# Kernel tuning notes

Measured on AMD Instinct MI355X. Metric: run time of the kernel, lower is better.

## Reference

```python
import jax, jax.numpy as jnp
import numpy as np

# Poincare ball hyperbolic multi-head attention (hypll-style HMultiheadAttention)
C = 1.0          # ball curvature
SQRT_C = 1.0
EPS = 1e-7
B, S, E, H = 4, 1024, 512, 8
HD = E // H      # head_dim = 64


def _project_to_ball(u, scale=0.5):
    n = jnp.linalg.norm(u, axis=-1, keepdims=True)
    return u * (scale / (1.0 + n))  # guarantees ||x|| < scale < 1/sqrt(C)


def h_linear(x, z, r):
    """Poincare fully-connected layer (Shimizu et al. HNN++), as in hypll HLinear.
    x: [..., n] points in the ball, z: [n, m] weight directions, r: [m] bias."""
    x2 = jnp.sum(x * x, -1, keepdims=True)
    lam = 2.0 / jnp.maximum(1.0 - C * x2, EPS)          # conformal factor lambda_x
    zn = jnp.maximum(jnp.linalg.norm(z, axis=0), EPS)    # [m]
    xz = x @ z                                           # [..., m]
    two_cr = 2.0 * SQRT_C * r
    v = (2.0 * zn / SQRT_C) * jnp.arcsinh(
        SQRT_C * lam * xz / zn * jnp.cosh(two_cr) - (lam - 1.0) * jnp.sinh(two_cr)
    )
    v2 = jnp.sum(v * v, -1, keepdims=True)
    return v / (1.0 + jnp.sqrt(1.0 + C * v2))            # map back into the ball


def _split_heads(x):
    b, s, e = x.shape
    return x.reshape(b, s, H, HD).transpose(0, 2, 1, 3)  # [B,H,S,hd]; matches split(dim=-1)


def _h_attention(q, k, v):
    # similarity = -poincare_dist(q, k), pairwise via the arccosh closed form
    # (avoids materializing a [B,H,Sq,Sk,hd] mobius_add tensor)
    q2 = jnp.sum(q * q, -1)[..., :, None]                # [B,H,Sq,1]
    k2 = jnp.sum(k * k, -1)[..., None, :]                # [B,H,1,Sk]
    qk = jnp.einsum('bhqd,bhkd->bhqk', q, k)
    diff2 = jnp.maximum(q2 + k2 - 2.0 * qk, 0.0)
    denom = jnp.maximum((1.0 - C * q2) * (1.0 - C * k2), EPS)
    arg = 1.0 + 2.0 * C * diff2 / denom
    dist = jnp.arccosh(jnp.maximum(arg, 1.0 + EPS)) / SQRT_C
    w = jax.nn.softmax(-dist, axis=-1)                   # attention_activation
    # attention_midpoint: weighted Mobius gyromidpoint then half scalar-mul
    v2 = jnp.sum(v * v, -1)                              # [B,H,Sk]
    lam = 2.0 / jnp.maximum(1.0 - C * v2, EPS)
    num = jnp.einsum('bhqk,bhkd->bhqd', w * lam[..., None, :], v)
    den = jnp.einsum('bhqk,bhk->bhq', w, lam - 1.0)[..., None]
    m_bar = num / jnp.where(jnp.abs(den) < EPS, EPS, den)
    mn = jnp.maximum(jnp.linalg.norm(m_bar, axis=-1, keepdims=True), EPS)
    t = jnp.minimum(SQRT_C * mn, 1.0 - 1e-6)
    return jnp.tanh(0.5 * jnp.arctanh(t)) * m_bar / (SQRT_C * mn)  # (1/2) mobius-scalar-mul


def setup_inputs() -> dict:
    key = jax.random.key(0)
    ks = jax.random.split(key, 9)
    query = _project_to_ball(jax.random.normal(ks[0], (B, S, E), jnp.float32))
    key_t = _project_to_ball(jax.random.normal(ks[1], (B, S, E), jnp.float32))
    value = _project_to_ball(jax.random.normal(ks[2], (B, S, E), jnp.float32))
    scale = E ** -0.5
    zq = jax.random.normal(ks[3], (E, E), jnp.float32) * scale
    zk = jax.random.normal(ks[4], (E, E), jnp.float32) * scale
    zv = jax.random.normal(ks[5], (E, E), jnp.float32) * scale
    rq = jax.random.normal(ks[6], (E,), jnp.float32) * 0.01
    rk = jax.random.normal(ks[7], (E,), jnp.float32) * 0.01
    rv = jax.random.normal(ks[8], (E,), jnp.float32) * 0.01
    return {"query": query, "key": key_t, "value": value,
            "zq": zq, "rq": rq, "zk": zk, "rk": rk, "zv": zv, "rv": rv}


def reference(query, key, value, zq, rq, zk, rk, zv, rv):
    pq = h_linear(query, zq, rq)
    pk = h_linear(key, zk, rk)
    pv = h_linear(value, zv, rv)
    q, k, v = _split_heads(pq), _split_heads(pk), _split_heads(pv)
    out = _h_attention(q, k, v)                          # [B,H,S,hd]
    return out.transpose(0, 2, 1, 3).reshape(B, S, E)    # manifold.cat over heads
```

## Files before the change

### kernel.cpp

```cpp
#include <hip/hip_runtime.h>
#include <math.h>

#define EPSf 1e-7f
typedef unsigned short u16;
typedef __attribute__((ext_vector_type(8))) short bf16x8;
typedef __attribute__((ext_vector_type(4))) float f32x4;

__device__ __forceinline__ float bf2f(u16 u) {
  union { unsigned int i; float f; } x; x.i = ((unsigned int)u) << 16; return x.f;
}
__device__ __forceinline__ u16 f2bf(float f) {
  union { float f; unsigned int i; } x; x.f = f;
  unsigned int r = x.i + 0x7fffu + ((x.i >> 16) & 1u);
  return (u16)(r >> 16);
}
__device__ __forceinline__ void gll16(const void* g, void* l) {
  __builtin_amdgcn_global_load_lds((__attribute__((address_space(1))) void*)(g),
                                   (__attribute__((address_space(3))) void*)(l),
                                   16, 0, 0);
}

__global__ __launch_bounds__(256) void split_z(
    const float* __restrict__ zq, const float* __restrict__ zk, const float* __restrict__ zv,
    const float* __restrict__ rq, const float* __restrict__ rk, const float* __restrict__ rv,
    u16* __restrict__ ZhT, u16* __restrict__ ZlT, float4* __restrict__ WM) {
  const int mat = blockIdx.x >> 3;
  const int c0 = (blockIdx.x & 7) * 64;
  const float* Z = (mat == 0) ? zq : (mat == 1) ? zk : zv;
  const float* R = (mat == 0) ? rq : (mat == 1) ? rk : rv;
  __shared__ float tile[64][68];
  const int t = threadIdx.x;
  const int cl = t >> 2, kg4 = t & 3;
  const size_t zo = (size_t)mat * 512 * 512;
  float csum = 0.f;
  for (int kt = 0; kt < 8; ++kt) {
    __syncthreads();
    {
      int kl = t >> 2;
      const float* src = Z + (size_t)(kt * 64 + kl) * 512 + c0;
      #pragma unroll
      for (int j = 0; j < 4; ++j) {
        float4 v = *(const float4*)(src + (t & 3) * 16 + 4 * j);
        *(float4*)&tile[kl][(t & 3) * 16 + 4 * j] = v;
      }
    }
    __syncthreads();
    #pragma unroll
    for (int jj = 0; jj < 4; ++jj) {
      u16 hb[4], lb[4];
      #pragma unroll
      for (int qq = 0; qq < 4; ++qq) {
        float zval = tile[kg4 * 16 + jj * 4 + qq][cl];
        csum = fmaf(zval, zval, csum);
        u16 hh = f2bf(zval);
        hb[qq] = hh;
        lb[qq] = f2bf(zval - bf2f(hh));
      }
      size_t o = zo + (size_t)(c0 + cl) * 512 + kt * 64 + kg4 * 16 + jj * 4;
      *(ushort4*)(ZhT + o) = make_ushort4(hb[0], hb[1], hb[2], hb[3]);
      *(ushort4*)(ZlT + o) = make_ushort4(lb[0], lb[1], lb[2], lb[3]);
    }
  }
  csum += __shfl_xor(csum, 1);
  csum += __shfl_xor(csum, 2);
  if (kg4 == 0) {
    float zn = fmaxf(sqrtf(csum), EPSf);
    float tr = 2.f * R[c0 + cl];
    float e = expf(tr), ei = 1.f / e;
    WM[mat * 512 + c0 + cl] = make_float4(0.5f * (e + ei) / zn, 0.5f * (e - ei), 2.f * zn, 0.f);
  }
}

__global__ __launch_bounds__(256) void split_x(
    const float* __restrict__ xq, const float* __restrict__ xk, const float* __restrict__ xv,
    u16* __restrict__ Xh, u16* __restrict__ Xl,
    float* __restrict__ Xn, float* __restrict__ Vn) {
  const int gr = blockIdx.x * 2 + (threadIdx.x >> 7);
  const int mat = gr >> 12, row = gr & 4095;
  const float* X = (mat == 0) ? xq : (mat == 1) ? xk : xv;
  const int f4 = threadIdx.x & 127;
  float4 x = ((const float4*)(X + (size_t)row * 512))[f4];
  u16 h0 = f2bf(x.x), h1 = f2bf(x.y), h2 = f2bf(x.z), h3 = f2bf(x.w);
  u16 l0 = f2bf(x.x - bf2f(h0)), l1 = f2bf(x.y - bf2f(h1));
  u16 l2 = f2bf(x.z - bf2f(h2)), l3 = f2bf(x.w - bf2f(h3));
  ((ushort4*)(Xh + (size_t)gr * 512))[f4] = make_ushort4(h0, h1, h2, h3);
  ((ushort4*)(Xl + (size_t)gr * 512))[f4] = make_ushort4(l0, l1, l2, l3);
  float a = fmaf(x.x, x.x, fmaf(x.y, x.y, fmaf(x.z, x.z, x.w * x.w)));
  a += __shfl_xor(a, 1);  a += __shfl_xor(a, 2);  a += __shfl_xor(a, 4);
  a += __shfl_xor(a, 8);  a += __shfl_xor(a, 16); a += __shfl_xor(a, 32);
  __shared__ float red[4];
  if ((threadIdx.x & 63) == 0) red[threadIdx.x >> 6] = a;
  __syncthreads();
  if (threadIdx.x == 0)   { Xn[gr] = red[0] + red[1]; Vn[gr] = 0.f; }
  if (threadIdx.x == 128) { Xn[gr] = red[2] + red[3]; Vn[gr] = 0.f; }
}

__global__ __launch_bounds__(256) void proj_gemm(
    const u16* __restrict__ Xh, const u16* __restrict__ Xl,
    const u16* __restrict__ ZhT, const u16* __restrict__ ZlT,
    const float* __restrict__ Xn, const float4* __restrict__ WM,
    float* __restrict__ Vtmp, float* __restrict__ Vn) {
  const int m0 = blockIdx.x * 128;
  const int n0 = blockIdx.y * 128;
  const int mat = blockIdx.z;
  const size_t xoff = (size_t)mat * 4096 * 512;
  const size_t zoff = (size_t)mat * 512 * 512;
  const int t = threadIdx.x, wv = t >> 6, lane = t & 63;
  const int l15 = lane & 15, quad = lane >> 4;

  __shared__ __align__(16) u16 Ah[128 * 32], Al[128 * 32], Bh[128 * 32], Bl[128 * 32];
  __shared__ float lams[128], lam1s[128], wmxs[128], wmys[128], wmzs[128];

  if (t < 128) {
    float x2 = Xn[mat * 4096 + m0 + t];
    float lam = 2.f / fmaxf(1.f - x2, EPSf);
    lams[t] = lam; lam1s[t] = lam - 1.f;
    float4 wm = WM[mat * 512 + n0 + t];
    wmxs[t] = wm.x; wmys[t] = wm.y; wmzs[t] = wm.z;
  }

  f32x4 acc[4][4];
  #pragma unroll
  for (int i = 0; i < 4; ++i)
    #pragma unroll
    for (int j = 0; j < 4; ++j) acc[i][j] = (f32x4){0.f, 0.f, 0.f, 0.f};

  const int srow = 32 * wv + (lane >> 2);
  const int scol = (lane & 3) * 8;
  const u16* gAh = Xh + xoff + (size_t)(m0 + srow) * 512 + scol;
  const u16* gAl = Xl + xoff + (size_t)(m0 + srow) * 512 + scol;
  const u16* gBh = ZhT + zoff + (size_t)(n0 + srow) * 512 + scol;
  const u16* gBl = ZlT + zoff + (size_t)(n0 + srow) * 512 + scol;

  for (int k0 = 0; k0 < 512; k0 += 32) {
    __syncthreads();
    gll16(gAh + k0,            &Ah[(32 * wv) * 32]);
    gll16(gAh + k0 + 16 * 512, &Ah[(32 * wv + 16) * 32]);
    gll16(gAl + k0,            &Al[(32 * wv) * 32]);
    gll16(gAl + k0 + 16 * 512, &Al[(32 * wv + 16) * 32]);
    gll16(gBh + k0,            &Bh[(32 * wv) * 32]);
    gll16(gBh + k0 + 16 * 512, &Bh[(32 * wv + 16) * 32]);
    gll16(gBl + k0,            &Bl[(32 * wv) * 32]);
    gll16(gBl + k0 + 16 * 512, &Bl[(32 * wv + 16) * 32]);
    __syncthreads();
    const int mh = (wv >> 1) * 64, nh = (wv & 1) * 64;
    bf16x8 ah[4], al[4], bh_[4], bl_[4];
    #pragma unroll
    for (int i = 0; i < 4; ++i) {
      int ra = mh + i * 16 + l15;
      ah[i] = *(const bf16x8*)&Ah[ra * 32 + quad * 8];
      al[i] = *(const bf16x8*)&Al[ra * 32 + quad * 8];
      int rb = nh + i * 16 + l15;
      bh_[i] = *(const bf16x8*)&Bh[rb * 32 + quad * 8];
      bl_[i] = *(const bf16x8*)&Bl[rb * 32 + quad * 8];
    }
    #pragma unroll
    for (int i = 0; i < 4; ++i)
      #pragma unroll
      for (int j = 0; j < 4; ++j) {
        acc[i][j] = __builtin_amdgcn_mfma_f32_16x16x32_bf16(ah[i], bh_[j], acc[i][j], 0, 0, 0);
        acc[i][j] = __builtin_amdgcn_mfma_f32_16x16x32_bf16(ah[i], bl_[j], acc[i][j], 0, 0, 0);
        acc[i][j] = __builtin_amdgcn_mfma_f32_16x16x32_bf16(al[i], bh_[j], acc[i][j], 0, 0, 0);
      }
  }

  const int mh = (wv >> 1) * 64, nh = (wv & 1) * 64;
  #pragma unroll
  for (int i = 0; i < 4; ++i) {
    float rsum[4] = {0.f, 0.f, 0.f, 0.f};
    #pragma unroll
    for (int j = 0; j < 4; ++j) {
      int nl = nh + j * 16 + l15;
      float wx = wmxs[nl], wy = wmys[nl], wz = wmzs[nl];
      #pragma unroll
      for (int r = 0; r < 4; ++r) {
        int ml = mh + i * 16 + quad * 4 + r;
        float tt = lams[ml] * acc[i][j][r] * wx - lam1s[ml] * wy;
        float v = wz * logf(tt + sqrtf(fmaf(tt, tt, 1.f)));
        Vtmp[xoff + (size_t)(m0 + ml) * 512 + (n0 + nl)] = v;
        rsum[r] = fmaf(v, v, rsum[r]);
      }
    }
    #pragma unroll
    for (int r = 0; r < 4; ++r) {
      rsum[r] += __shfl_xor(rsum[r], 1);
      rsum[r] += __shfl_xor(rsum[r], 2);
      rsum[r] += __shfl_xor(rsum[r], 4);
      rsum[r] += __shfl_xor(rsum[r], 8);
    }
    if (l15 == 0) {
      #pragma unroll
      for (int r = 0; r < 4; ++r)
        atomicAdd(&Vn[mat * 4096 + m0 + mh + i * 16 + quad * 4 + r], rsum[r]);
    }
  }
}

__global__ __launch_bounds__(256) void pack_qk(
    const float* __restrict__ Vtmp, const float* __restrict__ Vn,
    u16* __restrict__ Qh, u16* __restrict__ Kh,
    float* __restrict__ q2a, float* __restrict__ aqa,
    float* __restrict__ k2a, float* __restrict__ cka) {
  const int mat = blockIdx.x >> 7;
  const int rb = blockIdx.x & 127;
  const int r = threadIdx.x >> 3;
  const int h = threadIdx.x & 7;
  const int row = rb * 32 + r;
  const size_t gr = (size_t)mat * 4096 + row;
  const float sc = 1.f / (1.f + sqrtf(1.f + Vn[gr]));
  const float* src = Vtmp + gr * 512 + h * 64;
  const int b = row >> 10, s = row & 1023;
  u16* dst = (mat ? Kh : Qh) + ((size_t)(b * 8 + h) * 1024 + s) * 64;
  float nrm = 0.f;
  #pragma unroll
  for (int j = 0; j < 16; ++j) {
    float4 x = *(const float4*)(src + 4 * j);
    u16 u0 = f2bf(x.x * sc), u1 = f2bf(x.y * sc), u2 = f2bf(x.z * sc), u3 = f2bf(x.w * sc);
    *(ushort4*)(dst + 4 * j) = make_ushort4(u0, u1, u2, u3);
    float f0 = bf2f(u0), f1 = bf2f(u1), f2 = bf2f(u2), f3 = bf2f(u3);
    nrm += f0 * f0 + f1 * f1 + f2 * f2 + f3 * f3;
  }
  const size_t so = (size_t)(b * 8 + h) * 1024 + s;
  if (mat == 0) { q2a[so] = nrm; aqa[so] = 1.f / fmaxf(1.f - nrm, EPSf); }
  else          { k2a[so] = nrm; cka[so] = 2.f / fmaxf(1.f - nrm, EPSf); }
}

__global__ __launch_bounds__(256) void pack_v(
    const float* __restrict__ Vtmp, const float* __restrict__ Vn,
    u16* __restrict__ VTb, float* __restrict__ l1a) {
  const int bh = blockIdx.x >> 4;
  const int st = blockIdx.x & 15;
  const int b = bh >> 3, h = bh & 7;
  __shared__ u16 tile[64][72];
  __shared__ float lams[64];
  const int t = threadIdx.x;
  {
    const int s = t >> 2, dg = t & 3;
    const size_t gr = (size_t)2 * 4096 + b * 1024 + st * 64 + s;
    const float sc = 1.f / (1.f + sqrtf(1.f + Vn[gr]));
    const float* src = Vtmp + gr * 512 + h * 64 + dg * 16;
    float nrm = 0.f;
    #pragma unroll
    for (int j = 0; j < 4; ++j) {
      float4 x = *(const float4*)(src + 4 * j);
      u16 u0 = f2bf(x.x * sc), u1 = f2bf(x.y * sc), u2 = f2bf(x.z * sc), u3 = f2bf(x.w * sc);
      *(ushort4*)&tile[s][dg * 16 + 4 * j] = make_ushort4(u0, u1, u2, u3);
      float f0 = bf2f(u0), f1 = bf2f(u1), f2 = bf2f(u2), f3 = bf2f(u3);
      nrm += f0 * f0 + f1 * f1 + f2 * f2 + f3 * f3;
    }
    nrm += __shfl_xor(nrm, 1);
    nrm += __shfl_xor(nrm, 2);
    if (dg == 0) {
      float lam = 2.f / fmaxf(1.f - nrm, EPSf);
      lams[s] = lam;
      l1a[(size_t)bh * 1024 + st * 64 + s] = lam - 1.f;
    }
  }
  __syncthreads();
  const int d = t >> 2, sg = t & 3;
  u16 ob[16];
  #pragma unroll
  for (int j = 0; j < 16; ++j) {
    int ss = sg * 16 + j;
    ob[j] = f2bf(bf2f(tile[ss][d]) * lams[ss]);
  }
  u16* dst = VTb + ((size_t)bh * 64 + d) * 1024 + st * 64 + sg * 16;
  #pragma unroll
  for (int j = 0; j < 4; ++j)
    *(ushort4*)(dst + 4 * j) = make_ushort4(ob[4 * j], ob[4 * j + 1], ob[4 * j + 2], ob[4 * j + 3]);
}

__global__ __launch_bounds__(256) void attn(
    const u16* __restrict__ Qh, const u16* __restrict__ Kh, const u16* __restrict__ VTb,
    const float* __restrict__ q2a, const float* __restrict__ aqa,
    const float* __restrict__ k2a, const float* __restrict__ cka,
    const float* __restrict__ l1a, float* __restrict__ out) {
  const int bh = blockIdx.y;
  const int b = bh >> 3, h = bh & 7;
  const int q0 = blockIdx.x * 64;
  const int t = threadIdx.x, wv = t >> 6, lane = t & 63;
  const int l15 = lane & 15, quad = lane >> 4;

  __shared__ __align__(16) u16 Qs[64 * 72], Ks[64 * 72], VsT[64 * 72], Ws[64 * 72];
  __shared__ float k2s[64], cks[64], l1s[64], dens[64];

  #pragma unroll
  for (int i = 0; i < 2; ++i) {
    int f = t + 256 * i;
    int row = f >> 3, g = f & 7;
    float4 v = *(const float4*)(Qh + ((size_t)bh * 1024 + q0 + row) * 64 + g * 8);
    *(float4*)&Qs[row * 72 + g * 8] = v;
  }
  float q2r[4], aqr[4];
  #pragma unroll
  for (int r = 0; r < 4; ++r) {
    int qi = bh * 1024 + q0 + 16 * wv + 4 * quad + r;
    q2r[r] = q2a[qi];
    aqr[r] = aqa[qi];
  }
  __syncthreads();
  const bf16x8 qf0 = *(const bf16x8*)&Qs[(16 * wv + l15) * 72 + quad * 8];
  const bf16x8 qf1 = *(const bf16x8*)&Qs[(16 * wv + l15) * 72 + 32 + quad * 8];

  f32x4 num[4];
  #pragma unroll
  for (int i = 0; i < 4; ++i) num[i] = (f32x4){0.f, 0.f, 0.f, 0.f};
  float denp[4] = {0.f, 0.f, 0.f, 0.f};

  for (int kt = 0; kt < 16; ++kt) {
    __syncthreads();
    #pragma unroll
    for (int i = 0; i < 2; ++i) {
      int f = t + 256 * i;
      int row = f >> 3, g = f & 7;
      float4 kv = *(const float4*)(Kh + ((size_t)bh * 1024 + kt * 64 + row) * 64 + g * 8);
      *(float4*)&Ks[row * 72 + g * 8] = kv;
      float4 vv = *(const float4*)(VTb + ((size_t)bh * 64 + row) * 1024 + kt * 64 + g * 8);
      *(float4*)&VsT[row * 72 + g * 8] = vv;
    }
    if (t < 64) {
      int ki = bh * 1024 + kt * 64 + t;
      k2s[t] = k2a[ki]; cks[t] = cka[ki]; l1s[t] = l1a[ki];
    }
    __syncthreads();

    f32x4 sc_[4];
    #pragma unroll
    for (int tn = 0; tn < 4; ++tn) {
      bf16x8 kf0 = *(const bf16x8*)&Ks[(16 * tn + l15) * 72 + quad * 8];
      bf16x8 kf1 = *(const bf16x8*)&Ks[(16 * tn + l15) * 72 + 32 + quad * 8];
      f32x4 s = (f32x4){0.f, 0.f, 0.f, 0.f};
      s = __builtin_amdgcn_mfma_f32_16x16x32_bf16(qf0, kf0, s, 0, 0, 0);
      s = __builtin_amdgcn_mfma_f32_16x16x32_bf16(qf1, kf1, s, 0, 0, 0);
      sc_[tn] = s;
    }
    #pragma unroll
    for (int tn = 0; tn < 4; ++tn) {
      int kidx = 16 * tn + l15;
      float k2 = k2s[kidx], ck = cks[kidx], l1f = l1s[kidx];
      u16 wu[4];
      #pragma unroll
      for (int r = 0; r < 4; ++r) {
        float d2 = fmaxf(fmaf(-2.f, sc_[tn][r], q2r[r] + k2), 0.f);
        float u = fmaxf(d2 * ck * aqr[r], EPSf);
        float s2 = sqrtf(u * (u + 2.f));
        float w = (1.f + u) - s2;
        u16 wb = f2bf(w);
        wu[r] = wb;
        denp[r] = fmaf(bf2f(wb), l1f, denp[r]);
      }
      #pragma unroll
      for (int r = 0; r < 4; ++r)
        Ws[(16 * wv + 4 * quad + r) * 72 + kidx] = wu[r];
    }
    #pragma unroll
    for (int ks = 0; ks < 2; ++ks) {
      bf16x8 wf = *(const bf16x8*)&Ws[(16 * wv + l15) * 72 + ks * 32 + quad * 8];
      #pragma unroll
      for (int tm = 0; tm < 4; ++tm) {
        bf16x8 vf = *(const bf16x8*)&VsT[(16 * tm + l15) * 72 + ks * 32 + quad * 8];
        num[tm] = __builtin_amdgcn_mfma_f32_16x16x32_bf16(vf, wf, num[tm], 0, 0, 0);
      }
    }
  }

  #pragma unroll
  for (int r = 0; r < 4; ++r) {
    denp[r] += __shfl_xor(denp[r], 1);
    denp[r] += __shfl_xor(denp[r], 2);
    denp[r] += __shfl_xor(denp[r], 4);
    denp[r] += __shfl_xor(denp[r], 8);
  }
  if (l15 < 4) {
    float dv = (l15 == 0) ? denp[0] : (l15 == 1) ? denp[1] : (l15 == 2) ? denp[2] : denp[3];
    dens[16 * wv + 4 * quad + l15] = dv;
  }
  float den = dens[16 * wv + l15];
  den = (fabsf(den) < EPSf) ? EPSf : den;
  float inv = 1.f / den;
  float mv[4][4];
  float p = 0.f;
  #pragma unroll
  for (int tm = 0; tm < 4; ++tm)
    #pragma unroll
    for (int r = 0; r < 4; ++r) {
      float m = num[tm][r] * inv;
      mv[tm][r] = m;
      p = fmaf(m, m, p);
    }
  p += __shfl_xor(p, 16);
  p += __shfl_xor(p, 32);
  float mn = sqrtf(p);
  float mnc = fmaxf(mn, EPSf);
  float tt2 = fminf(mnc, 1.f - 1e-6f);
  float scale = tt2 / ((1.f + sqrtf(fmaxf(1.f - tt2 * tt2, 0.f))) * mnc);
  const int qg = b * 1024 + q0 + 16 * wv + l15;
  #pragma unroll
  for (int tm = 0; tm < 4; ++tm) {
    float4 o = make_float4(mv[tm][0] * scale, mv[tm][1] * scale, mv[tm][2] * scale, mv[tm][3] * scale);
    *(float4*)(out + (size_t)qg * 512 + h * 64 + tm * 16 + quad * 4) = o;
  }
}

extern "C" void kernel_launch(void* const* d_in, const int* in_sizes, int n_in,
                              void* d_out, int out_size, void* d_ws, size_t ws_size,
                              hipStream_t stream) {
  (void)in_sizes; (void)n_in; (void)out_size; (void)ws_size;
  const float* q  = (const float*)d_in[0];
  const float* k  = (const float*)d_in[1];
  const float* v  = (const float*)d_in[2];
  const float* zq = (const float*)d_in[3];
  const float* rq = (const float*)d_in[4];
  const float* zk = (const float*)d_in[5];
  const float* rk = (const float*)d_in[6];
  const float* zv = (const float*)d_in[7];
  const float* rv = (const float*)d_in[8];

  unsigned char* ws = (unsigned char*)d_ws;
  u16*   Xh   = (u16*)(ws + 0);
  u16*   Xl   = (u16*)(ws + 12582912);
  u16*   ZhT  = (u16*)(ws + 25165824);
  u16*   ZlT  = (u16*)(ws + 26738688);
  float* Vtmp = (float*)(ws + 28311552);
  float* Xn   = (float*)(ws + 53477376);
  float* Vn   = (float*)(ws + 53526528);
  float4* WM  = (float4*)(ws + 53575680);
  u16*   Qh   = (u16*)(ws + 0);
  u16*   Kh   = (u16*)(ws + 4194304);
  u16*   VTb  = (u16*)(ws + 8388608);
  float* q2a  = (float*)(ws + 12582912);
  float* aqa  = (float*)(ws + 12713984);
  float* k2a  = (float*)(ws + 12845056);
  float* cka  = (float*)(ws + 12976128);
  float* l1a  = (float*)(ws + 13107200);

  split_z<<<24, 256, 0, stream>>>(zq, zk, zv, rq, rk, rv, ZhT, ZlT, WM);
  split_x<<<6144, 256, 0, stream>>>(q, k, v, Xh, Xl, Xn, Vn);
  proj_gemm<<<dim3(32, 4, 3), 256, 0, stream>>>(Xh, Xl, ZhT, ZlT, Xn, WM, Vtmp, Vn);
  pack_qk<<<256, 256, 0, stream>>>(Vtmp, Vn, Qh, Kh, q2a, aqa, k2a, cka);
  pack_v<<<512, 256, 0, stream>>>(Vtmp, Vn, VTb, l1a);
  attn<<<dim3(16, 32), 256, 0, stream>>>(Qh, Kh, VTb, q2a, aqa, k2a, cka, l1a, (float*)d_out);
}
```

Measured before the change: 191.0 us.

## Raise grid parallelism across split_z, projection GEMM and attention; merge pack kernels

split_z now runs 192 blocks, one per k-tile, and accumulates column norms with atomics into a buffer zeroed by split_x. The WM bias terms are computed inside proj_gemm instead. proj_gemm uses 64-row tiles to double its block count, and pack_qk and pack_v merge into a single launch with the per-key scalars interleaved into a float4 array. attn switches to 32-query blocks that split the key range across wave pairs and reduce num and den through shared memory. All of this aims to fill more CUs on small grids and cut launch count, at the cost of atomics, extra shared-memory reductions and more redundant B-tile loads.

```diff
diff --git a/kernel.cpp b/kernel.cpp
--- a/kernel.cpp
+++ b/kernel.cpp
@@ -20,61 +20,14 @@
                                    16, 0, 0);
 }
 
-__global__ __launch_bounds__(256) void split_z(
-    const float* __restrict__ zq, const float* __restrict__ zk, const float* __restrict__ zv,
-    const float* __restrict__ rq, const float* __restrict__ rk, const float* __restrict__ rv,
-    u16* __restrict__ ZhT, u16* __restrict__ ZlT, float4* __restrict__ WM) {
-  const int mat = blockIdx.x >> 3;
-  const int c0 = (blockIdx.x & 7) * 64;
-  const float* Z = (mat == 0) ? zq : (mat == 1) ? zk : zv;
-  const float* R = (mat == 0) ? rq : (mat == 1) ? rk : rv;
-  __shared__ float tile[64][68];
-  const int t = threadIdx.x;
-  const int cl = t >> 2, kg4 = t & 3;
-  const size_t zo = (size_t)mat * 512 * 512;
-  float csum = 0.f;
-  for (int kt = 0; kt < 8; ++kt) {
-    __syncthreads();
-    {
-      int kl = t >> 2;
-      const float* src = Z + (size_t)(kt * 64 + kl) * 512 + c0;
-      #pragma unroll
-      for (int j = 0; j < 4; ++j) {
-        float4 v = *(const float4*)(src + (t & 3) * 16 + 4 * j);
-        *(float4*)&tile[kl][(t & 3) * 16 + 4 * j] = v;
-      }
-    }
-    __syncthreads();
-    #pragma unroll
-    for (int jj = 0; jj < 4; ++jj) {
-      u16 hb[4], lb[4];
-      #pragma unroll
-      for (int qq = 0; qq < 4; ++qq) {
-        float zval = tile[kg4 * 16 + jj * 4 + qq][cl];
-        csum = fmaf(zval, zval, csum);
-        u16 hh = f2bf(zval);
-        hb[qq] = hh;
-        lb[qq] = f2bf(zval - bf2f(hh));
-      }
-      size_t o = zo + (size_t)(c0 + cl) * 512 + kt * 64 + kg4 * 16 + jj * 4;
-      *(ushort4*)(ZhT + o) = make_ushort4(hb[0], hb[1], hb[2], hb[3]);
-      *(ushort4*)(ZlT + o) = make_ushort4(lb[0], lb[1], lb[2], lb[3]);
-    }
-  }
-  csum += __shfl_xor(csum, 1);
-  csum += __shfl_xor(csum, 2);
-  if (kg4 == 0) {
-    float zn = fmaxf(sqrtf(csum), EPSf);
-    float tr = 2.f * R[c0 + cl];
-    float e = expf(tr), ei = 1.f / e;
-    WM[mat * 512 + c0 + cl] = make_float4(0.5f * (e + ei) / zn, 0.5f * (e - ei), 2.f * zn, 0.f);
-  }
-}
-
 __global__ __launch_bounds__(256) void split_x(
     const float* __restrict__ xq, const float* __restrict__ xk, const float* __restrict__ xv,
     u16* __restrict__ Xh, u16* __restrict__ Xl,
-    float* __restrict__ Xn, float* __restrict__ Vn) {
+    float* __restrict__ Xn, float* __restrict__ Vn, float* __restrict__ Zn) {
+  if (blockIdx.x == 0) {
+    #pragma unroll
+    for (int j = 0; j < 6; ++j) Zn[threadIdx.x + 256 * j] = 0.f;
+  }
   const int gr = blockIdx.x * 2 + (threadIdx.x >> 7);
   const int mat = gr >> 12, row = gr & 4095;
   const float* X = (mat == 0) ? xq : (mat == 1) ? xk : xv;
@@ -95,67 +48,122 @@
   if (threadIdx.x == 128) { Xn[gr] = red[2] + red[3]; Vn[gr] = 0.f; }
 }
 
+__global__ __launch_bounds__(256) void split_z(
+    const float* __restrict__ zq, const float* __restrict__ zk, const float* __restrict__ zv,
+    u16* __restrict__ ZhT, u16* __restrict__ ZlT, float* __restrict__ Zn) {
+  const int idx = blockIdx.x;
+  const int mat = idx >> 6;
+  const int cg = (idx >> 3) & 7, kt = idx & 7;
+  const int c0 = cg * 64;
+  const float* Z = (mat == 0) ? zq : (mat == 1) ? zk : zv;
+  __shared__ float tile[64][68];
+  const int t = threadIdx.x;
+  {
+    int kl = t >> 2;
+    const float* src = Z + (size_t)(kt * 64 + kl) * 512 + c0 + (t & 3) * 16;
+    #pragma unroll
+    for (int j = 0; j < 4; ++j) {
+      float4 v = *(const float4*)(src + 4 * j);
+      *(float4*)&tile[kl][(t & 3) * 16 + 4 * j] = v;
+    }
+  }
+  __syncthreads();
+  const int cl = t >> 2, kg4 = t & 3;
+  const size_t zo = (size_t)mat * 512 * 512;
+  float csum = 0.f;
+  #pragma unroll
+  for (int jj = 0; jj < 4; ++jj) {
+    u16 hb[4], lb[4];
+    #pragma unroll
+    for (int qq = 0; qq < 4; ++qq) {
+      float zval = tile[kg4 * 16 + jj * 4 + qq][cl];
+      csum = fmaf(zval, zval, csum);
+      u16 hh = f2bf(zval);
+      hb[qq] = hh;
+      lb[qq] = f2bf(zval - bf2f(hh));
+    }
+    size_t o = zo + (size_t)(c0 + cl) * 512 + kt * 64 + kg4 * 16 + jj * 4;
+    *(ushort4*)(ZhT + o) = make_ushort4(hb[0], hb[1], hb[2], hb[3]);
+    *(ushort4*)(ZlT + o) = make_ushort4(lb[0], lb[1], lb[2], lb[3]);
+  }
+  csum += __shfl_xor(csum, 1);
+  csum += __shfl_xor(csum, 2);
+  if (kg4 == 0) atomicAdd(&Zn[mat * 512 + c0 + cl], csum);
+}
+
 __global__ __launch_bounds__(256) void proj_gemm(
     const u16* __restrict__ Xh, const u16* __restrict__ Xl,
     const u16* __restrict__ ZhT, const u16* __restrict__ ZlT,
-    const float* __restrict__ Xn, const float4* __restrict__ WM,
+    const float* __restrict__ Xn, const float* __restrict__ Zn,
+    const float* __restrict__ rq, const float* __restrict__ rk, const float* __restrict__ rv,
     float* __restrict__ Vtmp, float* __restrict__ Vn) {
-  const int m0 = blockIdx.x * 128;
+  const int m0 = blockIdx.x * 64;
   const int n0 = blockIdx.y * 128;
   const int mat = blockIdx.z;
   const size_t xoff = (size_t)mat * 4096 * 512;
   const size_t zoff = (size_t)mat * 512 * 512;
   const int t = threadIdx.x, wv = t >> 6, lane = t & 63;
   const int l15 = lane & 15, quad = lane >> 4;
-
-  __shared__ __align__(16) u16 Ah[128 * 32], Al[128 * 32], Bh[128 * 32], Bl[128 * 32];
-  __shared__ float lams[128], lam1s[128], wmxs[128], wmys[128], wmzs[128];
-
-  if (t < 128) {
+  const int wm = wv >> 1, wn = wv & 1;
+
+  __shared__ __align__(16) u16 SM[12288];
+  __shared__ float lams[64], lam1s[64], wmxs[128], wmys[128], wmzs[128];
+
+  if (t < 64) {
     float x2 = Xn[mat * 4096 + m0 + t];
     float lam = 2.f / fmaxf(1.f - x2, EPSf);
     lams[t] = lam; lam1s[t] = lam - 1.f;
-    float4 wm = WM[mat * 512 + n0 + t];
-    wmxs[t] = wm.x; wmys[t] = wm.y; wmzs[t] = wm.z;
-  }
-
-  f32x4 acc[4][4];
-  #pragma unroll
-  for (int i = 0; i < 4; ++i)
+  }
+  if (t < 128) {
+    float zn = fmaxf(sqrtf(Zn[mat * 512 + n0 + t]), EPSf);
+    const float* R = (mat == 0) ? rq : (mat == 1) ? rk : rv;
+    float tr = 2.f * R[n0 + t];
+    float e = expf(tr), ei = 1.f / e;
+    wmxs[t] = 0.5f * (e + ei) / zn;
+    wmys[t] = 0.5f * (e - ei);
+    wmzs[t] = 2.f * zn;
+  }
+
+  f32x4 acc[2][4];
+  #pragma unroll
+  for (int i = 0; i < 2; ++i)
     #pragma unroll
     for (int j = 0; j < 4; ++j) acc[i][j] = (f32x4){0.f, 0.f, 0.f, 0.f};
 
-  const int srow = 32 * wv + (lane >> 2);
-  const int scol = (lane & 3) * 8;
-  const u16* gAh = Xh + xoff + (size_t)(m0 + srow) * 512 + scol;
-  const u16* gAl = Xl + xoff + (size_t)(m0 + srow) * 512 + scol;
-  const u16* gBh = ZhT + zoff + (size_t)(n0 + srow) * 512 + scol;
-  const u16* gBl = ZlT + zoff + (size_t)(n0 + srow) * 512 + scol;
+  const u16* gs[6];
+  u16* ld[6];
+  #pragma unroll
+  for (int ci = 0; ci < 6; ++ci) {
+    int c = wv + 4 * ci;
+    const u16* arr; int row0, lo;
+    if (c < 4)       { arr = Xh + xoff;  row0 = m0 + 16 * c;        lo = c * 512; }
+    else if (c < 8)  { arr = Xl + xoff;  row0 = m0 + 16 * (c - 4);  lo = 2048 + (c - 4) * 512; }
+    else if (c < 16) { arr = ZhT + zoff; row0 = n0 + 16 * (c - 8);  lo = 4096 + (c - 8) * 512; }
+    else             { arr = ZlT + zoff; row0 = n0 + 16 * (c - 16); lo = 8192 + (c - 16) * 512; }
+    gs[ci] = arr + (size_t)(row0 + (lane >> 2)) * 512 + (lane & 3) * 8;
+    ld[ci] = SM + lo;
+  }
 
   for (int k0 = 0; k0 < 512; k0 += 32) {
     __syncthreads();
-    gll16(gAh + k0,            &Ah[(32 * wv) * 32]);
-    gll16(gAh + k0 + 16 * 512, &Ah[(32 * wv + 16) * 32]);
-    gll16(gAl + k0,            &Al[(32 * wv) * 32]);
-    gll16(gAl + k0 + 16 * 512, &Al[(32 * wv + 16) * 32]);
-    gll16(gBh + k0,            &Bh[(32 * wv) * 32]);
-    gll16(gBh + k0 + 16 * 512, &Bh[(32 * wv + 16) * 32]);
-    gll16(gBl + k0,            &Bl[(32 * wv) * 32]);
-    gll16(gBl + k0 + 16 * 512, &Bl[(32 * wv + 16) * 32]);
+    #pragma unroll
+    for (int ci = 0; ci < 6; ++ci) gll16(gs[ci] + k0, ld[ci]);
     __syncthreads();
-    const int mh = (wv >> 1) * 64, nh = (wv & 1) * 64;
-    bf16x8 ah[4], al[4], bh_[4], bl_[4];
-    #pragma unroll
-    for (int i = 0; i < 4; ++i) {
-      int ra = mh + i * 16 + l15;
-      ah[i] = *(const bf16x8*)&Ah[ra * 32 + quad * 8];
-      al[i] = *(const bf16x8*)&Al[ra * 32 + quad * 8];
-      int rb = nh + i * 16 + l15;
-      bh_[i] = *(const bf16x8*)&Bh[rb * 32 + quad * 8];
-      bl_[i] = *(const bf16x8*)&Bl[rb * 32 + quad * 8];
-    }
-    #pragma unroll
-    for (int i = 0; i < 4; ++i)
+    bf16x8 ah[2], al[2], bh_[4], bl_[4];
+    #pragma unroll
+    for (int i = 0; i < 2; ++i) {
+      int ra = wm * 32 + i * 16 + l15;
+      ah[i] = *(const bf16x8*)&SM[ra * 32 + quad * 8];
+      al[i] = *(const bf16x8*)&SM[2048 + ra * 32 + quad * 8];
+    }
+    #pragma unroll
+    for (int j = 0; j < 4; ++j) {
+      int rb = wn * 64 + j * 16 + l15;
+      bh_[j] = *(const bf16x8*)&SM[4096 + rb * 32 + quad * 8];
+      bl_[j] = *(const bf16x8*)&SM[8192 + rb * 32 + quad * 8];
+    }
+    #pragma unroll
+    for (int i = 0; i < 2; ++i)
       #pragma unroll
       for (int j = 0; j < 4; ++j) {
         acc[i][j] = __builtin_amdgcn_mfma_f32_16x16x32_bf16(ah[i], bh_[j], acc[i][j], 0, 0, 0);
@@ -164,17 +172,16 @@
       }
   }
 
-  const int mh = (wv >> 1) * 64, nh = (wv & 1) * 64;
-  #pragma unroll
-  for (int i = 0; i < 4; ++i) {
+  #pragma unroll
+  for (int i = 0; i < 2; ++i) {
     float rsum[4] = {0.f, 0.f, 0.f, 0.f};
     #pragma unroll
     for (int j = 0; j < 4; ++j) {
-      int nl = nh + j * 16 + l15;
+      int nl = wn * 64 + j * 16 + l15;
       float wx = wmxs[nl], wy = wmys[nl], wz = wmzs[nl];
       #pragma unroll
       for (int r = 0; r < 4; ++r) {
-        int ml = mh + i * 16 + quad * 4 + r;
+        int ml = wm * 32 + i * 16 + quad * 4 + r;
         float tt = lams[ml] * acc[i][j][r] * wx - lam1s[ml] * wy;
         float v = wz * logf(tt + sqrtf(fmaf(tt, tt, 1.f)));
         Vtmp[xoff + (size_t)(m0 + ml) * 512 + (n0 + nl)] = v;
@@ -191,116 +198,117 @@
     if (l15 == 0) {
       #pragma unroll
       for (int r = 0; r < 4; ++r)
-        atomicAdd(&Vn[mat * 4096 + m0 + mh + i * 16 + quad * 4 + r], rsum[r]);
-    }
-  }
-}
-
-__global__ __launch_bounds__(256) void pack_qk(
+        atomicAdd(&Vn[mat * 4096 + m0 + wm * 32 + i * 16 + quad * 4 + r], rsum[r]);
+    }
+  }
+}
+
+__global__ __launch_bounds__(256) void pack(
     const float* __restrict__ Vtmp, const float* __restrict__ Vn,
-    u16* __restrict__ Qh, u16* __restrict__ Kh,
-    float* __restrict__ q2a, float* __restrict__ aqa,
-    float* __restrict__ k2a, float* __restrict__ cka) {
-  const int mat = blockIdx.x >> 7;
-  const int rb = blockIdx.x & 127;
-  const int r = threadIdx.x >> 3;
-  const int h = threadIdx.x & 7;
-  const int row = rb * 32 + r;
-  const size_t gr = (size_t)mat * 4096 + row;
-  const float sc = 1.f / (1.f + sqrtf(1.f + Vn[gr]));
-  const float* src = Vtmp + gr * 512 + h * 64;
-  const int b = row >> 10, s = row & 1023;
-  u16* dst = (mat ? Kh : Qh) + ((size_t)(b * 8 + h) * 1024 + s) * 64;
-  float nrm = 0.f;
-  #pragma unroll
-  for (int j = 0; j < 16; ++j) {
-    float4 x = *(const float4*)(src + 4 * j);
-    u16 u0 = f2bf(x.x * sc), u1 = f2bf(x.y * sc), u2 = f2bf(x.z * sc), u3 = f2bf(x.w * sc);
-    *(ushort4*)(dst + 4 * j) = make_ushort4(u0, u1, u2, u3);
-    float f0 = bf2f(u0), f1 = bf2f(u1), f2 = bf2f(u2), f3 = bf2f(u3);
-    nrm += f0 * f0 + f1 * f1 + f2 * f2 + f3 * f3;
-  }
-  const size_t so = (size_t)(b * 8 + h) * 1024 + s;
-  if (mat == 0) { q2a[so] = nrm; aqa[so] = 1.f / fmaxf(1.f - nrm, EPSf); }
-  else          { k2a[so] = nrm; cka[so] = 2.f / fmaxf(1.f - nrm, EPSf); }
-}
-
-__global__ __launch_bounds__(256) void pack_v(
-    const float* __restrict__ Vtmp, const float* __restrict__ Vn,
-    u16* __restrict__ VTb, float* __restrict__ l1a) {
-  const int bh = blockIdx.x >> 4;
-  const int st = blockIdx.x & 15;
-  const int b = bh >> 3, h = bh & 7;
+    u16* __restrict__ Qh, u16* __restrict__ Kh, u16* __restrict__ VTb,
+    float* __restrict__ q2a, float* __restrict__ aqa, float4* __restrict__ ksc) {
   __shared__ u16 tile[64][72];
   __shared__ float lams[64];
   const int t = threadIdx.x;
-  {
-    const int s = t >> 2, dg = t & 3;
-    const size_t gr = (size_t)2 * 4096 + b * 1024 + st * 64 + s;
+  if (blockIdx.x < 256) {
+    const int mat = blockIdx.x >> 7;
+    const int rb = blockIdx.x & 127;
+    const int r = t >> 3, h = t & 7;
+    const int row = rb * 32 + r;
+    const size_t gr = (size_t)mat * 4096 + row;
     const float sc = 1.f / (1.f + sqrtf(1.f + Vn[gr]));
-    const float* src = Vtmp + gr * 512 + h * 64 + dg * 16;
+    const float* src = Vtmp + gr * 512 + h * 64;
+    const int b = row >> 10, s = row & 1023;
+    u16* dst = (mat ? Kh : Qh) + ((size_t)(b * 8 + h) * 1024 + s) * 64;
     float nrm = 0.f;
     #pragma unroll
-    for (int j = 0; j < 4; ++j) {
+    for (int j = 0; j < 16; ++j) {
       float4 x = *(const float4*)(src + 4 * j);
       u16 u0 = f2bf(x.x * sc), u1 = f2bf(x.y * sc), u2 = f2bf(x.z * sc), u3 = f2bf(x.w * sc);
-      *(ushort4*)&tile[s][dg * 16 + 4 * j] = make_ushort4(u0, u1, u2, u3);
+      *(ushort4*)(dst + 4 * j) = make_ushort4(u0, u1, u2, u3);
       float f0 = bf2f(u0), f1 = bf2f(u1), f2 = bf2f(u2), f3 = bf2f(u3);
       nrm += f0 * f0 + f1 * f1 + f2 * f2 + f3 * f3;
     }
-    nrm += __shfl_xor(nrm, 1);
-    nrm += __shfl_xor(nrm, 2);
-    if (dg == 0) {
-      float lam = 2.f / fmaxf(1.f - nrm, EPSf);
-      lams[s] = lam;
-      l1a[(size_t)bh * 1024 + st * 64 + s] = lam - 1.f;
-    }
-  }
-  __syncthreads();
-  const int d = t >> 2, sg = t & 3;
-  u16 ob[16];
-  #pragma unroll
-  for (int j = 0; j < 16; ++j) {
-    int ss = sg * 16 + j;
-    ob[j] = f2bf(bf2f(tile[ss][d]) * lams[ss]);
-  }
-  u16* dst = VTb + ((size_t)bh * 64 + d) * 1024 + st * 64 + sg * 16;
-  #pragma unroll
-  for (int j = 0; j < 4; ++j)
-    *(ushort4*)(dst + 4 * j) = make_ushort4(ob[4 * j], ob[4 * j + 1], ob[4 * j + 2], ob[4 * j + 3]);
+    const size_t so = (size_t)(b * 8 + h) * 1024 + s;
+    if (mat == 0) { q2a[so] = nrm; aqa[so] = 1.f / fmaxf(1.f - nrm, EPSf); }
+    else {
+      float2 kk = make_float2(nrm, 2.f / fmaxf(1.f - nrm, EPSf));
+      *(float2*)&ksc[so] = kk;
+    }
+  } else {
+    const int idx = blockIdx.x - 256;
+    const int bh = idx >> 4, st = idx & 15;
+    const int b = bh >> 3, h = bh & 7;
+    {
+      const int s = t >> 2, dg = t & 3;
+      const size_t gr = (size_t)2 * 4096 + b * 1024 + st * 64 + s;
+      const float sc = 1.f / (1.f + sqrtf(1.f + Vn[gr]));
+      const float* src = Vtmp + gr * 512 + h * 64 + dg * 16;
+      float nrm = 0.f;
+      #pragma unroll
+      for (int j = 0; j < 4; ++j) {
+        float4 x = *(const float4*)(src + 4 * j);
+        u16 u0 = f2bf(x.x * sc), u1 = f2bf(x.y * sc), u2 = f2bf(x.z * sc), u3 = f2bf(x.w * sc);
+        *(ushort4*)&tile[s][dg * 16 + 4 * j] = make_ushort4(u0, u1, u2, u3);
+        float f0 = bf2f(u0), f1 = bf2f(u1), f2 = bf2f(u2), f3 = bf2f(u3);
+        nrm += f0 * f0 + f1 * f1 + f2 * f2 + f3 * f3;
+      }
+      nrm += __shfl_xor(nrm, 1);
+      nrm += __shfl_xor(nrm, 2);
+      if (dg == 0) {
+        float lam = 2.f / fmaxf(1.f - nrm, EPSf);
+        lams[s] = lam;
+        ((float*)&ksc[(size_t)bh * 1024 + st * 64 + s])[3] = lam - 1.f;
+      }
+    }
+    __syncthreads();
+    const int d = t >> 2, sg = t & 3;
+    u16 ob[16];
+    #pragma unroll
+    for (int j = 0; j < 16; ++j) {
+      int ss = sg * 16 + j;
+      ob[j] = f2bf(bf2f(tile[ss][d]) * lams[ss]);
+    }
+    u16* dst = VTb + ((size_t)bh * 64 + d) * 1024 + st * 64 + sg * 16;
+    #pragma unroll
+    for (int j = 0; j < 4; ++j)
+      *(ushort4*)(dst + 4 * j) = make_ushort4(ob[4 * j], ob[4 * j + 1], ob[4 * j + 2], ob[4 * j + 3]);
+  }
 }
 
 __global__ __launch_bounds__(256) void attn(
     const u16* __restrict__ Qh, const u16* __restrict__ Kh, const u16* __restrict__ VTb,
     const float* __restrict__ q2a, const float* __restrict__ aqa,
-    const float* __restrict__ k2a, const float* __restrict__ cka,
-    const float* __restrict__ l1a, float* __restrict__ out) {
+    const float4* __restrict__ ksc, float* __restrict__ out) {
   const int bh = blockIdx.y;
   const int b = bh >> 3, h = bh & 7;
-  const int q0 = blockIdx.x * 64;
+  const int q0 = blockIdx.x * 32;
   const int t = threadIdx.x, wv = t >> 6, lane = t & 63;
   const int l15 = lane & 15, quad = lane >> 4;
-
-  __shared__ __align__(16) u16 Qs[64 * 72], Ks[64 * 72], VsT[64 * 72], Ws[64 * 72];
-  __shared__ float k2s[64], cks[64], l1s[64], dens[64];
-
-  #pragma unroll
-  for (int i = 0; i < 2; ++i) {
-    int f = t + 256 * i;
-    int row = f >> 3, g = f & 7;
+  const int qh = wv >> 1, kh = wv & 1;
+
+  __shared__ __align__(16) u16 Qs[32 * 72];
+  __shared__ __align__(16) u16 Ks[64 * 72];
+  __shared__ __align__(16) u16 VsT[64 * 72];
+  __shared__ __align__(16) u16 Ws[4 * 16 * 36];
+  __shared__ float dens[64];
+  __shared__ __align__(16) float nums[2][16][68];
+
+  {
+    int row = t >> 3, g = t & 7;
     float4 v = *(const float4*)(Qh + ((size_t)bh * 1024 + q0 + row) * 64 + g * 8);
     *(float4*)&Qs[row * 72 + g * 8] = v;
   }
   float q2r[4], aqr[4];
   #pragma unroll
   for (int r = 0; r < 4; ++r) {
-    int qi = bh * 1024 + q0 + 16 * wv + 4 * quad + r;
+    int qi = bh * 1024 + q0 + qh * 16 + quad * 4 + r;
     q2r[r] = q2a[qi];
     aqr[r] = aqa[qi];
   }
   __syncthreads();
-  const bf16x8 qf0 = *(const bf16x8*)&Qs[(16 * wv + l15) * 72 + quad * 8];
-  const bf16x8 qf1 = *(const bf16x8*)&Qs[(16 * wv + l15) * 72 + 32 + quad * 8];
+  const bf16x8 qf0 = *(const bf16x8*)&Qs[(qh * 16 + l15) * 72 + quad * 8];
+  const bf16x8 qf1 = *(const bf16x8*)&Qs[(qh * 16 + l15) * 72 + 32 + quad * 8];
 
   f32x4 num[4];
   #pragma unroll
@@ -309,58 +317,51 @@
 
   for (int kt = 0; kt < 16; ++kt) {
     __syncthreads();
-    #pragma unroll
-    for (int i = 0; i < 2; ++i) {
-      int f = t + 256 * i;
-      int row = f >> 3, g = f & 7;
-      float4 kv = *(const float4*)(Kh + ((size_t)bh * 1024 + kt * 64 + row) * 64 + g * 8);
-      *(float4*)&Ks[row * 72 + g * 8] = kv;
-      float4 vv = *(const float4*)(VTb + ((size_t)bh * 64 + row) * 1024 + kt * 64 + g * 8);
-      *(float4*)&VsT[row * 72 + g * 8] = vv;
-    }
-    if (t < 64) {
-      int ki = bh * 1024 + kt * 64 + t;
-      k2s[t] = k2a[ki]; cks[t] = cka[ki]; l1s[t] = l1a[ki];
+    {
+      int row = t >> 3, g = t & 7;
+      #pragma unroll
+      for (int p = 0; p < 2; ++p) {
+        int rr = row + 32 * p;
+        float4 kv = *(const float4*)(Kh + ((size_t)bh * 1024 + kt * 64 + rr) * 64 + g * 8);
+        *(float4*)&Ks[rr * 72 + g * 8] = kv;
+        float4 vvv = *(const float4*)(VTb + ((size_t)bh * 64 + rr) * 1024 + kt * 64 + g * 8);
+        *(float4*)&VsT[rr * 72 + g * 8] = vvv;
+      }
     }
     __syncthreads();
 
-    f32x4 sc_[4];
-    #pragma unroll
-    for (int tn = 0; tn < 4; ++tn) {
-      bf16x8 kf0 = *(const bf16x8*)&Ks[(16 * tn + l15) * 72 + quad * 8];
-      bf16x8 kf1 = *(const bf16x8*)&Ks[(16 * tn + l15) * 72 + 32 + quad * 8];
-      f32x4 s = (f32x4){0.f, 0.f, 0.f, 0.f};
-      s = __builtin_amdgcn_mfma_f32_16x16x32_bf16(qf0, kf0, s, 0, 0, 0);
-      s = __builtin_amdgcn_mfma_f32_16x16x32_bf16(qf1, kf1, s, 0, 0, 0);
-      sc_[tn] = s;
-    }
-    #pragma unroll
-    for (int tn = 0; tn < 4; ++tn) {
-      int kidx = 16 * tn + l15;
-      float k2 = k2s[kidx], ck = cks[kidx], l1f = l1s[kidx];
-      u16 wu[4];
+    f32x4 s0 = (f32x4){0.f, 0.f, 0.f, 0.f};
+    f32x4 s1 = (f32x4){0.f, 0.f, 0.f, 0.f};
+    {
+      const bf16x8 ka0 = *(const bf16x8*)&Ks[(kh * 32 + l15) * 72 + quad * 8];
+      const bf16x8 ka1 = *(const bf16x8*)&Ks[(kh * 32 + l15) * 72 + 32 + quad * 8];
+      const bf16x8 kb0 = *(const bf16x8*)&Ks[(kh * 32 + 16 + l15) * 72 + quad * 8];
+      const bf16x8 kb1 = *(const bf16x8*)&Ks[(kh * 32 + 16 + l15) * 72 + 32 + quad * 8];
+      s0 = __builtin_amdgcn_mfma_f32_16x16x32_bf16(qf0, ka0, s0, 0, 0, 0);
+      s0 = __builtin_amdgcn_mfma_f32_16x16x32_bf16(qf1, ka1, s0, 0, 0, 0);
+      s1 = __builtin_amdgcn_mfma_f32_16x16x32_bf16(qf0, kb0, s1, 0, 0, 0);
+      s1 = __builtin_amdgcn_mfma_f32_16x16x32_bf16(qf1, kb1, s1, 0, 0, 0);
+    }
+    #pragma unroll
+    for (int tn = 0; tn < 2; ++tn) {
+      float4 kv = ksc[(size_t)bh * 1024 + kt * 64 + kh * 32 + tn * 16 + l15];
+      float k2 = kv.x, ck = kv.y, l1f = kv.w;
+      f32x4 s = tn ? s1 : s0;
       #pragma unroll
       for (int r = 0; r < 4; ++r) {
-        float d2 = fmaxf(fmaf(-2.f, sc_[tn][r], q2r[r] + k2), 0.f);
+        float d2 = fmaxf(fmaf(-2.f, s[r], q2r[r] + k2), 0.f);
         float u = fmaxf(d2 * ck * aqr[r], EPSf);
-        float s2 = sqrtf(u * (u + 2.f));
-        float w = (1.f + u) - s2;
+        float w = (1.f + u) - sqrtf(u * (u + 2.f));
         u16 wb = f2bf(w);
-        wu[r] = wb;
         denp[r] = fmaf(bf2f(wb), l1f, denp[r]);
-      }
-      #pragma unroll
-      for (int r = 0; r < 4; ++r)
-        Ws[(16 * wv + 4 * quad + r) * 72 + kidx] = wu[r];
-    }
-    #pragma unroll
-    for (int ks = 0; ks < 2; ++ks) {
-      bf16x8 wf = *(const bf16x8*)&Ws[(16 * wv + l15) * 72 + ks * 32 + quad * 8];
-      #pragma unroll
-      for (int tm = 0; tm < 4; ++tm) {
-        bf16x8 vf = *(const bf16x8*)&VsT[(16 * tm + l15) * 72 + ks * 32 + quad * 8];
-        num[tm] = __builtin_amdgcn_mfma_f32_16x16x32_bf16(vf, wf, num[tm], 0, 0, 0);
-      }
+        Ws[wv * 576 + (quad * 4 + r) * 36 + tn * 16 + l15] = wb;
+      }
+    }
+    const bf16x8 wf = *(const bf16x8*)&Ws[wv * 576 + l15 * 36 + quad * 8];
+    #pragma unroll
+    for (int tm = 0; tm < 4; ++tm) {
+      const bf16x8 vf = *(const bf16x8*)&VsT[(tm * 16 + l15) * 72 + kh * 32 + quad * 8];
+      num[tm] = __builtin_amdgcn_mfma_f32_16x16x32_bf16(vf, wf, num[tm], 0, 0, 0);
     }
   }
 
@@ -371,34 +372,49 @@
     denp[r] += __shfl_xor(denp[r], 4);
     denp[r] += __shfl_xor(denp[r], 8);
   }
-  if (l15 < 4) {
-    float dv = (l15 == 0) ? denp[0] : (l15 == 1) ? denp[1] : (l15 == 2) ? denp[2] : denp[3];
-    dens[16 * wv + 4 * quad + l15] = dv;
-  }
-  float den = dens[16 * wv + l15];
-  den = (fabsf(den) < EPSf) ? EPSf : den;
-  float inv = 1.f / den;
-  float mv[4][4];
-  float p = 0.f;
-  #pragma unroll
-  for (int tm = 0; tm < 4; ++tm)
-    #pragma unroll
-    for (int r = 0; r < 4; ++r) {
-      float m = num[tm][r] * inv;
-      mv[tm][r] = m;
-      p = fmaf(m, m, p);
-    }
-  p += __shfl_xor(p, 16);
-  p += __shfl_xor(p, 32);
-  float mn = sqrtf(p);
-  float mnc = fmaxf(mn, EPSf);
-  float tt2 = fminf(mnc, 1.f - 1e-6f);
-  float scale = tt2 / ((1.f + sqrtf(fmaxf(1.f - tt2 * tt2, 0.f))) * mnc);
-  const int qg = b * 1024 + q0 + 16 * wv + l15;
-  #pragma unroll
-  for (int tm = 0; tm < 4; ++tm) {
-    float4 o = make_float4(mv[tm][0] * scale, mv[tm][1] * scale, mv[tm][2] * scale, mv[tm][3] * scale);
-    *(float4*)(out + (size_t)qg * 512 + h * 64 + tm * 16 + quad * 4) = o;
+  if (l15 == 0) {
+    #pragma unroll
+    for (int r = 0; r < 4; ++r) dens[wv * 16 + quad * 4 + r] = denp[r];
+  }
+  if (kh == 1) {
+    #pragma unroll
+    for (int tm = 0; tm < 4; ++tm)
+      *(float4*)&nums[qh][l15][tm * 16 + quad * 4] =
+          make_float4(num[tm][0], num[tm][1], num[tm][2], num[tm][3]);
+  }
+  __syncthreads();
+  if (kh == 0) {
+    #pragma unroll
+    for (int tm = 0; tm < 4; ++tm) {
+      float4 o = *(const float4*)&nums[qh][l15][tm * 16 + quad * 4];
+      num[tm][0] += o.x; num[tm][1] += o.y; num[tm][2] += o.z; num[tm][3] += o.w;
+    }
+    float den = dens[qh * 32 + l15] + dens[qh * 32 + 16 + l15];
+    den = (fabsf(den) < EPSf) ? EPSf : den;
+    float inv = 1.f / den;
+    float mv[4][4];
+    float p = 0.f;
+    #pragma unroll
+    for (int tm = 0; tm < 4; ++tm)
+      #pragma unroll
+      for (int r = 0; r < 4; ++r) {
+        float m = num[tm][r] * inv;
+        mv[tm][r] = m;
+        p = fmaf(m, m, p);
+      }
+    p += __shfl_xor(p, 16);
+    p += __shfl_xor(p, 32);
+    float mn = sqrtf(p);
+    float mnc = fmaxf(mn, EPSf);
+    float tt2 = fminf(mnc, 1.f - 1e-6f);
+    float scale = tt2 / ((1.f + sqrtf(fmaxf(1.f - tt2 * tt2, 0.f))) * mnc);
+    const size_t qg = (size_t)b * 1024 + q0 + qh * 16 + l15;
+    #pragma unroll
+    for (int tm = 0; tm < 4; ++tm) {
+      float4 o = make_float4(mv[tm][0] * scale, mv[tm][1] * scale,
+                             mv[tm][2] * scale, mv[tm][3] * scale);
+      *(float4*)(out + qg * 512 + h * 64 + tm * 16 + quad * 4) = o;
+    }
   }
 }
 
@@ -424,20 +440,17 @@
   float* Vtmp = (float*)(ws + 28311552);
   float* Xn   = (float*)(ws + 53477376);
   float* Vn   = (float*)(ws + 53526528);
-  float4* WM  = (float4*)(ws + 53575680);
+  float* Zn   = (float*)(ws + 53575680);
   u16*   Qh   = (u16*)(ws + 0);
   u16*   Kh   = (u16*)(ws + 4194304);
   u16*   VTb  = (u16*)(ws + 8388608);
   float* q2a  = (float*)(ws + 12582912);
   float* aqa  = (float*)(ws + 12713984);
-  float* k2a  = (float*)(ws + 12845056);
-  float* cka  = (float*)(ws + 12976128);
-  float* l1a  = (float*)(ws + 13107200);
-
-  split_z<<<24, 256, 0, stream>>>(zq, zk, zv, rq, rk, rv, ZhT, ZlT, WM);
-  split_x<<<6144, 256, 0, stream>>>(q, k, v, Xh, Xl, Xn, Vn);
-  proj_gemm<<<dim3(32, 4, 3), 256, 0, stream>>>(Xh, Xl, ZhT, ZlT, Xn, WM, Vtmp, Vn);
-  pack_qk<<<256, 256, 0, stream>>>(Vtmp, Vn, Qh, Kh, q2a, aqa, k2a, cka);
-  pack_v<<<512, 256, 0, stream>>>(Vtmp, Vn, VTb, l1a);
-  attn<<<dim3(16, 32), 256, 0, stream>>>(Qh, Kh, VTb, q2a, aqa, k2a, cka, l1a, (float*)d_out);
-}
+  float4* ksc = (float4*)(ws + 12845056);
+
+  split_x<<<6144, 256, 0, stream>>>(q, k, v, Xh, Xl, Xn, Vn, Zn);
+  split_z<<<192, 256, 0, stream>>>(zq, zk, zv, ZhT, ZlT, Zn);
+  proj_gemm<<<dim3(64, 4, 3), 256, 0, stream>>>(Xh, Xl, ZhT, ZlT, Xn, Zn, rq, rk, rv, Vtmp, Vn);
+  pack<<<768, 256, 0, stream>>>(Vtmp, Vn, Qh, Kh, VTb, q2a, aqa, ksc);
+  attn<<<dim3(32, 32), 256, 0, stream>>>(Qh, Kh, VTb, q2a, aqa, ksc, (float*)d_out);
+}
```

New measurement: 182.7 us. -4.3%, faster.
